# Kernel tuning notes

Measured on AMD Instinct MI355X. Metric: run time of the kernel, lower is better.

Reference implementation:

```python
import jax, jax.numpy as jnp
import numpy as np

NUM_HEADS = 8      # SD1.x UNet cross-attn heads at 64x64 block
NUM_PROMPTS = 4    # batch = 2*NUM_PROMPTS (uncond + cond CFG halves)


def setup_inputs() -> dict:
    key = jax.random.key(0)
    ks = jax.random.split(key, 8)
    B, T, C = 2 * NUM_PROMPTS, 4096, 320   # spatial tokens, inner dim
    S, D = 77, 768                          # CLIP text seq len / width
    return {
        "hidden_states": jax.random.normal(ks[0], (B, T, C), jnp.float32),
        "encoder_hidden_states": jax.random.normal(ks[1], (B, S, D), jnp.float32),
        "mapper": jax.random.uniform(ks[2], (NUM_PROMPTS - 1, S, S), jnp.float32),
        "Wq": jax.random.normal(ks[3], (C, C), jnp.float32) * 0.02,
        "Wk": jax.random.normal(ks[4], (D, C), jnp.float32) * 0.02,
        "Wv": jax.random.normal(ks[5], (D, C), jnp.float32) * 0.02,
        "Wo": jax.random.normal(ks[6], (C, C), jnp.float32) * 0.02,
        "bo": jnp.zeros((C,), jnp.float32),
    }


def reference(hidden_states, encoder_hidden_states, mapper, Wq, Wk, Wv, Wo, bo):
    B, T, C = hidden_states.shape
    S = encoder_hidden_states.shape[1]
    H = NUM_HEADS
    d = C // H
    scale = 1.0 / jnp.sqrt(jnp.asarray(d, hidden_states.dtype))

    # projections + head split (diffusers head_to_batch_dim layout)
    q = (hidden_states @ Wq).reshape(B, T, H, d)
    k = (encoder_hidden_states @ Wk).reshape(B, S, H, d)
    v = (encoder_hidden_states @ Wv).reshape(B, S, H, d)

    # full attention probabilities must be materialized for the P2P swap
    scores = jnp.einsum('bthd,bshd->bhts', q, k) * scale
    probs = jax.nn.softmax(scores, axis=-1)  # [B, H, T, S]

    # conditional (CFG) half: [P, H, T, S]; swap via mapper einsum (cross-attn,
    # cur_step < num_steps_cross branch of swap_attention_probs)
    half = B // 2
    uncond = probs[:half]
    cond = probs[half:]
    attn_base = cond[0]                                   # [H, T, S]
    replaced = jnp.einsum('htm,pme->phte', attn_base, mapper)  # [P-1, H, T, S]
    cond = jnp.concatenate([attn_base[None], replaced], axis=0)
    probs = jnp.concatenate([uncond, cond], axis=0)

    # value matmul + merge heads (batch_to_head_dim) + output projection
    out = jnp.einsum('bhts,bshd->bthd', probs, v).reshape(B, T, C)
    return out @ Wo + bo
```

## Files before the change

kernel.cpp:

```cpp
#include <hip/hip_runtime.h>
#include <hip/hip_bf16.h>

typedef unsigned short ushort;
typedef __attribute__((ext_vector_type(8))) short bf16x8;
typedef __attribute__((ext_vector_type(8))) unsigned short ushort8;
typedef __attribute__((ext_vector_type(4))) float f32x4;
typedef __attribute__((ext_vector_type(4))) float float4v;

__device__ __forceinline__ ushort f2bf(float f) {
    union { float f; unsigned u; } v; v.f = f;
    unsigned r = v.u + 0x7FFFu + ((v.u >> 16) & 1u);
    return (ushort)(r >> 16);
}
__device__ __forceinline__ float bf2f(ushort u) {
    union { unsigned u; float f; } v; v.u = ((unsigned)u) << 16;
    return v.f;
}

#define KF_SZ   (5u * 8 * 5 * 2 * 512)
#define VF_SZ   (5u * 8 * 3 * 3 * 512)
#define VPF_SZ  (3u * 8 * 3 * 3 * 512)
#define WF_SZ   (10u * 2 * 10 * 512)

__global__ __launch_bounds__(256) void prep_k(
    const float* __restrict__ Wq, const float* __restrict__ Wk,
    const float* __restrict__ Wv, const float* __restrict__ Wo,
    ushort* __restrict__ Wq_t, ushort* __restrict__ Wk_t,
    ushort* __restrict__ Wv_t, ushort* __restrict__ Wo_t,
    ushort* __restrict__ Kf, ushort* __restrict__ Vf, ushort* __restrict__ VPf)
{
    int b = blockIdx.x;
    if (b >= 680) {
        const ushort8 z8 = {0,0,0,0,0,0,0,0};
        unsigned i = (b - 680) * 256 + threadIdx.x;
        if (i < KF_SZ / 8) ((ushort8*)Kf)[i] = z8;
        else if (i < (KF_SZ + VF_SZ) / 8) ((ushort8*)Vf)[i - KF_SZ / 8] = z8;
        else if (i < (KF_SZ + VF_SZ + VPF_SZ) / 8) ((ushort8*)VPf)[i - (KF_SZ + VF_SZ) / 8] = z8;
        return;
    }
    __shared__ ushort t[32][33];
    const float* src; ushort* dst; int K; int tb;
    if (b < 100)      { src = Wq; dst = Wq_t; K = 320; tb = b; }
    else if (b < 340) { src = Wk; dst = Wk_t; K = 768; tb = b - 100; }
    else if (b < 580) { src = Wv; dst = Wv_t; K = 768; tb = b - 340; }
    else              { src = Wo; dst = Wo_t; K = 320; tb = b - 580; }
    int tc = tb % 10, tr = tb / 10;
    int tx = threadIdx.x & 31, ty = threadIdx.x >> 5;
    #pragma unroll
    for (int p = 0; p < 4; ++p) {
        int k = tr * 32 + ty + p * 8, n = tc * 32 + tx;
        t[ty + p * 8][tx] = f2bf(src[(size_t)k * 320 + n]);
    }
    __syncthreads();
    #pragma unroll
    for (int p = 0; p < 4; ++p) {
        int n = tc * 32 + ty + p * 8, k = tr * 32 + tx;
        dst[(size_t)n * K + k] = t[tx][ty + p * 8];
    }
}

__global__ __launch_bounds__(256) void gemm_kv(
    const float* __restrict__ E, const ushort* __restrict__ Wk_t,
    const ushort* __restrict__ Wv_t, const ushort* __restrict__ Wq_t,
    const ushort* __restrict__ Wo_t,
    float* __restrict__ part, ushort* __restrict__ Wof, ushort* __restrict__ Wqf)
{
    const int tid = threadIdx.x;
    const int bid = blockIdx.x;
    if (bid >= 160) {
        int i = (bid - 160) * 256 + tid;
        const ushort* src; ushort* dst;
        if (i < 12800) { src = Wo_t; dst = Wof; }
        else           { src = Wq_t; dst = Wqf; i -= 12800; }
        int g = i >> 6, l = i & 63;
        int kk = g / 20, half = (g / 10) & 1, f = g % 10;
        int n = half * 160 + f * 16 + (l & 15);
        int k0 = kk * 32 + (l >> 4) * 8;
        *(ushort8*)(dst + (size_t)g * 512 + l * 8) =
            *(const ushort8*)(src + (size_t)n * 320 + k0);
        return;
    }
    __shared__ ushort A_lds[2][64 * 40];
    __shared__ ushort B_lds[2][320 * 40];
    const int w = tid >> 6, l = tid & 63;
    const int c15 = l & 15, khi = (l >> 4) * 8;
    const int r = tid >> 2, p = (tid & 3) * 8;
    const int rbase = (l >> 4) * 4;
    f32x4 acc[4][5] = {};

    const int mtile = bid % 10, mat = (bid / 10) & 1, ks = bid / 20;
    const int m0 = mtile * 64, kk0 = ks * 96;
    const ushort* Bt = mat ? Wv_t : Wk_t;
    const int m = m0 + r;
    const bool live = (m < 616);
    const float* Abase = E + (size_t)(live ? m : 0) * 768 + p;
    float4v a0 = {0,0,0,0}, a1 = {0,0,0,0};
    ushort8 breg[5];
    if (live) { a0 = *(const float4v*)(Abase + kk0); a1 = *(const float4v*)(Abase + kk0 + 4); }
    #pragma unroll
    for (int i = 0; i < 5; ++i) {
        int idx = tid + i * 256; int n = idx >> 2, q = (idx & 3) * 8;
        breg[i] = *(const ushort8*)(Bt + (size_t)n * 768 + kk0 + q);
    }
    {
        ushort* d = &A_lds[0][r * 40 + p];
        d[0]=f2bf(a0.x); d[1]=f2bf(a0.y); d[2]=f2bf(a0.z); d[3]=f2bf(a0.w);
        d[4]=f2bf(a1.x); d[5]=f2bf(a1.y); d[6]=f2bf(a1.z); d[7]=f2bf(a1.w);
        #pragma unroll
        for (int i = 0; i < 5; ++i) {
            int idx = tid + i * 256; int n = idx >> 2, q = (idx & 3) * 8;
            *(ushort8*)&B_lds[0][n * 40 + q] = breg[i];
        }
    }
    __syncthreads();
    for (int k = 0; k < 3; ++k) {
        const int cur = k & 1;
        if (k < 2) {
            int kk = kk0 + (k + 1) * 32;
            if (live) { a0 = *(const float4v*)(Abase + kk); a1 = *(const float4v*)(Abase + kk + 4); }
            #pragma unroll
            for (int i = 0; i < 5; ++i) {
                int idx = tid + i * 256; int n = idx >> 2, q = (idx & 3) * 8;
                breg[i] = *(const ushort8*)(Bt + (size_t)n * 768 + kk + q);
            }
        }
        bf16x8 a[4];
        #pragma unroll
        for (int mf = 0; mf < 4; ++mf)
            a[mf] = *(const bf16x8*)&A_lds[cur][(mf * 16 + c15) * 40 + khi];
        #pragma unroll
        for (int f = 0; f < 5; ++f) {
            bf16x8 b = *(const bf16x8*)&B_lds[cur][(w * 80 + f * 16 + c15) * 40 + khi];
            #pragma unroll
            for (int mf = 0; mf < 4; ++mf)
                acc[mf][f] = __builtin_amdgcn_mfma_f32_16x16x32_bf16(a[mf], b, acc[mf][f], 0, 0, 0);
        }
        if (k < 2) {
            const int nxt = cur ^ 1;
            ushort* d = &A_lds[nxt][r * 40 + p];
            d[0]=f2bf(a0.x); d[1]=f2bf(a0.y); d[2]=f2bf(a0.z); d[3]=f2bf(a0.w);
            d[4]=f2bf(a1.x); d[5]=f2bf(a1.y); d[6]=f2bf(a1.z); d[7]=f2bf(a1.w);
            #pragma unroll
            for (int i = 0; i < 5; ++i) {
                int idx = tid + i * 256; int n = idx >> 2, q = (idx & 3) * 8;
                *(ushort8*)&B_lds[nxt][n * 40 + q] = breg[i];
            }
            __syncthreads();
        }
    }
    float* dst = part + (size_t)(mat * 8 + ks) * 640 * 320;
    #pragma unroll
    for (int mf = 0; mf < 4; ++mf)
        #pragma unroll
        for (int f = 0; f < 5; ++f) {
            int col = w * 80 + f * 16 + c15;
            #pragma unroll
            for (int rr = 0; rr < 4; ++rr)
                dst[(size_t)(m0 + mf * 16 + rbase + rr) * 320 + col] = acc[mf][f][rr];
        }
}

__global__ __launch_bounds__(256) void kv_reduce(
    const float* __restrict__ part, ushort* __restrict__ Kf,
    ushort* __restrict__ Vf, ushort* __restrict__ VVt)
{
    int idx = blockIdx.x * 256 + threadIdx.x;
    if (idx >= 616 * 320) return;
    int mat = blockIdx.y;
    int row = idx / 320, col = idx - row * 320;
    float s8 = 0.f;
    #pragma unroll
    for (int ks = 0; ks < 8; ++ks)
        s8 += part[((size_t)(mat * 8 + ks) * 640 + row) * 320 + col];
    ushort b = f2bf(s8);
    int bt = row / 77, s = row - bt * 77;
    int h = col / 40, kd = col - h * 40;
    if (mat == 0) {
        if (bt < 5) {
            int kt = kd >> 5, chunk = (kd >> 3) & 3;
            int lane = (s & 15) | (chunk << 4);
            Kf[((size_t)((bt * 8 + h) * 5 + (s >> 4)) * 2 + kt) * 512 + lane * 8 + (kd & 7)] = b;
        }
    } else {
        if (bt < 5) {
            int lane = (kd & 15) | (((s >> 3) & 3) << 4);
            Vf[(((size_t)(bt * 8 + h) * 3 + (kd >> 4)) * 3 + (s >> 5)) * 512 + lane * 8 + (s & 7)] = b;
        } else {
            VVt[((size_t)bt * 320 + col) * 80 + s] = b;
        }
    }
}

__global__ void vprime_k(const float* __restrict__ mapper, const ushort* __restrict__ VVt,
                         ushort* __restrict__ VPf)
{
    int pm = blockIdx.x;
    int p = pm / 77, m = pm - p * 77;
    __shared__ float mp[77];
    int tid = threadIdx.x;
    if (tid < 77) mp[tid] = mapper[(size_t)pm * 77 + tid];
    __syncthreads();
    const ushort* vrow = VVt + ((size_t)(5 + p) * 320 + tid) * 80;
    float acc = 0.f;
    for (int e = 0; e < 77; ++e) acc += mp[e] * bf2f(vrow[e]);
    int h = tid / 40, dc = tid - h * 40;
    int lane = (dc & 15) | (((m >> 3) & 3) << 4);
    VPf[(((size_t)(p * 8 + h) * 3 + (dc >> 4)) * 3 + (m >> 5)) * 512 + lane * 8 + (m & 7)] = f2bf(acc);
}

#define ATT_SCALE 0.15811388300841897f
__global__ __launch_bounds__(512, 4) void attn_out_k(
    const float* __restrict__ hs, const ushort* __restrict__ Wqf,
    const ushort* __restrict__ Kf, const ushort* __restrict__ Vf,
    const ushort* __restrict__ VPf, const ushort* __restrict__ Wof,
    const float* __restrict__ bias, float* __restrict__ out)
{
    __shared__ __align__(16) ushort AO_lds[64 * 328];
    __shared__ __align__(16) ushort P_lds[8 * 16 * 104];
    ushort* W_lds = P_lds;

    const int tid = threadIdx.x;
    const int ww = tid >> 6, l = tid & 63;
    const int c15 = l & 15, hi4 = l >> 4;
    const int khi = hi4 * 8, rbase = hi4 * 4;
    const int bt = blockIdx.y, t0 = blockIdx.x * 64;
    const int qb = (bt < 5) ? bt : 4;
    const ushort* Vfb = (bt < 5) ? (Vf + (size_t)bt * (8 * 3 * 3 * 512))
                                 : (VPf + (size_t)(bt - 5) * (8 * 3 * 3 * 512));
    const ushort8 z8 = {0,0,0,0,0,0,0,0};
    ushort* Pw = P_lds + ww * (16 * 104);
    const int rg = ww & 3, half = ww >> 2;
    const int cb = half * 160;

    for (int i = tid; i < 2560; i += 512) {
        int r = i / 40, cc = i - (i / 40) * 40;
        const float4v* s = (const float4v*)(hs + (size_t)(qb * 4096 + t0 + r) * 320 + cc * 8);
        float4v x0 = s[0], x1 = s[1];
        ushort* d = &AO_lds[r * 328 + cc * 8];
        d[0]=f2bf(x0.x); d[1]=f2bf(x0.y); d[2]=f2bf(x0.z); d[3]=f2bf(x0.w);
        d[4]=f2bf(x1.x); d[5]=f2bf(x1.y); d[6]=f2bf(x1.z); d[7]=f2bf(x1.w);
    }
    __syncthreads();

    {
        f32x4 qacc[10] = {};
        for (int kk = 0; kk < 10; ++kk) {
            const ushort* wsrc = Wqf + (size_t)kk * 10240;
            int c0 = tid, c1 = tid + 512, c2 = tid + 1024;
            *(ushort8*)&W_lds[c0 * 8] = *(const ushort8*)(wsrc + c0 * 8);
            *(ushort8*)&W_lds[c1 * 8] = *(const ushort8*)(wsrc + c1 * 8);
            if (c2 < 1280) *(ushort8*)&W_lds[c2 * 8] = *(const ushort8*)(wsrc + c2 * 8);
            __syncthreads();
            bf16x8 a = *(const bf16x8*)&AO_lds[(rg * 16 + c15) * 328 + kk * 32 + khi];
            #pragma unroll
            for (int f = 0; f < 10; ++f) {
                bf16x8 b = *(const bf16x8*)&W_lds[(half * 10 + f) * 512 + l * 8];
                qacc[f] = __builtin_amdgcn_mfma_f32_16x16x32_bf16(a, b, qacc[f], 0, 0, 0);
            }
            __syncthreads();
        }
        #pragma unroll
        for (int f = 0; f < 10; ++f) {
            int col = cb + f * 16 + c15;
            #pragma unroll
            for (int rr = 0; rr < 4; ++rr)
                AO_lds[(rg * 16 + rbase + rr) * 328 + col] = f2bf(qacc[f][rr]);
        }
    }
    __syncthreads();

    const int h = ww;
    if (l < 48) {
        int r = l / 3, c = l - 3 * (l / 3);
        *(ushort8*)&Pw[r * 104 + 80 + c * 8] = z8;
    }
    bf16x8 kreg[5][2];
    #pragma unroll
    for (int f = 0; f < 5; ++f) {
        const ushort* kfb = Kf + ((size_t)((qb * 8 + h) * 5 + f) * 2) * 512 + l * 8;
        kreg[f][0] = *(const bf16x8*)(kfb);
        kreg[f][1] = *(const bf16x8*)(kfb + 512);
    }

    for (int rg4 = 0; rg4 < 4; ++rg4) {
        bf16x8 qa0 = *(const bf16x8*)&AO_lds[(rg4 * 16 + c15) * 328 + h * 40 + khi];
        bf16x8 qa1 = {0,0,0,0,0,0,0,0};
        if (hi4 == 0) qa1 = *(const bf16x8*)&AO_lds[(rg4 * 16 + c15) * 328 + h * 40 + 32];

        f32x4 sacc[5] = {};
        #pragma unroll
        for (int f = 0; f < 5; ++f) {
            sacc[f] = __builtin_amdgcn_mfma_f32_16x16x32_bf16(qa0, kreg[f][0], sacc[f], 0, 0, 0);
            sacc[f] = __builtin_amdgcn_mfma_f32_16x16x32_bf16(qa1, kreg[f][1], sacc[f], 0, 0, 0);
        }

        float pv[5][4];
        #pragma unroll
        for (int r = 0; r < 4; ++r) {
            float sum = 0.f;
            #pragma unroll
            for (int f = 0; f < 5; ++f) {
                bool valid = (f < 4) || (c15 < 13);
                float e = valid ? __expf(sacc[f][r] * ATT_SCALE) : 0.f;
                pv[f][r] = e; sum += e;
            }
            #pragma unroll
            for (int d = 1; d < 16; d <<= 1) sum += __shfl_xor(sum, d);
            float inv = 1.f / sum;
            #pragma unroll
            for (int f = 0; f < 5; ++f) pv[f][r] *= inv;
        }

        #pragma unroll
        for (int r = 0; r < 4; ++r)
            #pragma unroll
            for (int f = 0; f < 5; ++f)
                Pw[(rbase + r) * 104 + f * 16 + c15] = f2bf(pv[f][r]);

        bf16x8 pa[3];
        #pragma unroll
        for (int kt = 0; kt < 3; ++kt)
            pa[kt] = *(const bf16x8*)&Pw[c15 * 104 + kt * 32 + khi];
        f32x4 oacc[3];
        #pragma unroll
        for (int f = 0; f < 3; ++f) {
            bf16x8 v0 = *(const bf16x8*)(Vfb + (((size_t)(h * 3 + f) * 3 + 0)) * 512 + l * 8);
            bf16x8 v1 = *(const bf16x8*)(Vfb + (((size_t)(h * 3 + f) * 3 + 1)) * 512 + l * 8);
            bf16x8 v2 = *(const bf16x8*)(Vfb + (((size_t)(h * 3 + f) * 3 + 2)) * 512 + l * 8);
            f32x4 o = {};
            o = __builtin_amdgcn_mfma_f32_16x16x32_bf16(pa[0], v0, o, 0, 0, 0);
            o = __builtin_amdgcn_mfma_f32_16x16x32_bf16(pa[1], v1, o, 0, 0, 0);
            o = __builtin_amdgcn_mfma_f32_16x16x32_bf16(pa[2], v2, o, 0, 0, 0);
            oacc[f] = o;
        }

        #pragma unroll
        for (int f = 0; f < 3; ++f) {
            int col = f * 16 + c15;
            if (col < 40) {
                #pragma unroll
                for (int r = 0; r < 4; ++r)
                    AO_lds[(rg4 * 16 + rbase + r) * 328 + h * 40 + col] = f2bf(oacc[f][r]);
            }
        }
    }
    __syncthreads();

    f32x4 acc[10] = {};
    for (int kk = 0; kk < 10; ++kk) {
        const ushort* wsrc = Wof + (size_t)kk * 10240;
        {
            int c0 = tid, c1 = tid + 512, c2 = tid + 1024;
            *(ushort8*)&W_lds[c0 * 8] = *(const ushort8*)(wsrc + c0 * 8);
            *(ushort8*)&W_lds[c1 * 8] = *(const ushort8*)(wsrc + c1 * 8);
            if (c2 < 1280) *(ushort8*)&W_lds[c2 * 8] = *(const ushort8*)(wsrc + c2 * 8);
        }
        __syncthreads();
        bf16x8 a = *(const bf16x8*)&AO_lds[(rg * 16 + c15) * 328 + kk * 32 + khi];
        #pragma unroll
        for (int f = 0; f < 10; ++f) {
            bf16x8 b = *(const bf16x8*)&W_lds[(half * 10 + f) * 512 + l * 8];
            acc[f] = __builtin_amdgcn_mfma_f32_16x16x32_bf16(a, b, acc[f], 0, 0, 0);
        }
        if (kk < 9) __syncthreads();
    }

    #pragma unroll
    for (int f = 0; f < 10; ++f) {
        int col = cb + f * 16 + c15;
        #pragma unroll
        for (int rr = 0; rr < 4; ++rr)
            out[(size_t)(bt * 4096 + t0 + rg * 16 + rbase + rr) * 320 + col]
                = acc[f][rr] + bias[col];
    }
}

extern "C" void kernel_launch(void* const* d_in, const int* in_sizes, int n_in,
                              void* d_out, int out_size, void* d_ws, size_t ws_size,
                              hipStream_t stream) {
    (void)in_sizes; (void)n_in; (void)out_size; (void)ws_size;
    const float* hs     = (const float*)d_in[0];
    const float* ehs    = (const float*)d_in[1];
    const float* mapper = (const float*)d_in[2];
    const float* Wq     = (const float*)d_in[3];
    const float* Wk     = (const float*)d_in[4];
    const float* Wv     = (const float*)d_in[5];
    const float* Wo     = (const float*)d_in[6];
    const float* bo     = (const float*)d_in[7];
    float* out = (float*)d_out;

    ushort* ws   = (ushort*)d_ws;
    ushort* Wq_t = ws;
    ushort* Wk_t = Wq_t + 320 * 320;
    ushort* Wv_t = Wk_t + 320 * 768;
    ushort* Wo_t = Wv_t + 320 * 768;
    ushort* Wof  = Wo_t + 320 * 320;
    ushort* Wqf  = Wof + WF_SZ;
    ushort* Kfb  = Wqf + WF_SZ;
    ushort* Vfb  = Kfb + KF_SZ;
    ushort* VPfb = Vfb + VF_SZ;
    ushort* VVt  = VPfb + VPF_SZ;
    float*  part = (float*)(VVt + 8 * 320 * 80);

    prep_k<<<1069, 256, 0, stream>>>(Wq, Wk, Wv, Wo, Wq_t, Wk_t, Wv_t, Wo_t,
                                     Kfb, Vfb, VPfb);
    gemm_kv<<<260, 256, 0, stream>>>(ehs, Wk_t, Wv_t, Wq_t, Wo_t, part, Wof, Wqf);
    kv_reduce<<<dim3(770, 2), 256, 0, stream>>>(part, Kfb, Vfb, VVt);
    vprime_k<<<231, 320, 0, stream>>>(mapper, VVt, VPfb);
    attn_out_k<<<dim3(64, 8), 512, 0, stream>>>(hs, Wqf, Kfb, Vfb, VPfb, Wof, bo, out);
}
```

Measured before the change: 65.65 us.

## Load Q/O projection weights directly from global into registers, retile warps 2x4

The Q and output projection GEMMs no longer stage weight tiles through LDS with per-k barriers. Each warp now covers 32 rows by 80 columns, reading B fragments straight from global memory in a re-laid-out weight format and reusing each fragment across two row fragments. This removes 20 block-wide barriers and LDS traffic per projection. The cost is that weight reads now depend on L2/global latency with no LDS sharing across warps. The P padding zeroing is moved earlier because LDS is no longer reused for weights.

```diff
diff --git a/kernel.cpp b/kernel.cpp
--- a/kernel.cpp
+++ b/kernel.cpp
@@ -20,7 +20,7 @@
 #define KF_SZ   (5u * 8 * 5 * 2 * 512)
 #define VF_SZ   (5u * 8 * 3 * 3 * 512)
 #define VPF_SZ  (3u * 8 * 3 * 3 * 512)
-#define WF_SZ   (10u * 2 * 10 * 512)
+#define WF_SZ   (10u * 4 * 5 * 512)
 
 __global__ __launch_bounds__(256) void prep_k(
     const float* __restrict__ Wq, const float* __restrict__ Wk,
@@ -73,8 +73,8 @@
         if (i < 12800) { src = Wo_t; dst = Wof; }
         else           { src = Wq_t; dst = Wqf; i -= 12800; }
         int g = i >> 6, l = i & 63;
-        int kk = g / 20, half = (g / 10) & 1, f = g % 10;
-        int n = half * 160 + f * 16 + (l & 15);
+        int kk = g / 20, cg = (g / 5) & 3, f = g % 5;
+        int n = cg * 80 + f * 16 + (l & 15);
         int k0 = kk * 32 + (l >> 4) * 8;
         *(ushort8*)(dst + (size_t)g * 512 + l * 8) =
             *(const ushort8*)(src + (size_t)n * 320 + k0);
@@ -217,7 +217,6 @@
 {
     __shared__ __align__(16) ushort AO_lds[64 * 328];
     __shared__ __align__(16) ushort P_lds[8 * 16 * 104];
-    ushort* W_lds = P_lds;
 
     const int tid = threadIdx.x;
     const int ww = tid >> 6, l = tid & 63;
@@ -229,8 +228,12 @@
                                  : (VPf + (size_t)(bt - 5) * (8 * 3 * 3 * 512));
     const ushort8 z8 = {0,0,0,0,0,0,0,0};
     ushort* Pw = P_lds + ww * (16 * 104);
-    const int rg = ww & 3, half = ww >> 2;
-    const int cb = half * 160;
+    const int rp = ww & 1, cg = ww >> 1;
+
+    if (l < 48) {
+        int r = l / 3, c = l - 3 * (l / 3);
+        *(ushort8*)&Pw[r * 104 + 80 + c * 8] = z8;
+    }
 
     for (int i = tid; i < 2560; i += 512) {
         int r = i / 40, cc = i - (i / 40) * 40;
@@ -243,37 +246,32 @@
     __syncthreads();
 
     {
-        f32x4 qacc[10] = {};
+        f32x4 qacc[2][5] = {};
         for (int kk = 0; kk < 10; ++kk) {
-            const ushort* wsrc = Wqf + (size_t)kk * 10240;
-            int c0 = tid, c1 = tid + 512, c2 = tid + 1024;
-            *(ushort8*)&W_lds[c0 * 8] = *(const ushort8*)(wsrc + c0 * 8);
-            *(ushort8*)&W_lds[c1 * 8] = *(const ushort8*)(wsrc + c1 * 8);
-            if (c2 < 1280) *(ushort8*)&W_lds[c2 * 8] = *(const ushort8*)(wsrc + c2 * 8);
-            __syncthreads();
-            bf16x8 a = *(const bf16x8*)&AO_lds[(rg * 16 + c15) * 328 + kk * 32 + khi];
-            #pragma unroll
-            for (int f = 0; f < 10; ++f) {
-                bf16x8 b = *(const bf16x8*)&W_lds[(half * 10 + f) * 512 + l * 8];
-                qacc[f] = __builtin_amdgcn_mfma_f32_16x16x32_bf16(a, b, qacc[f], 0, 0, 0);
-            }
-            __syncthreads();
-        }
-        #pragma unroll
-        for (int f = 0; f < 10; ++f) {
-            int col = cb + f * 16 + c15;
-            #pragma unroll
-            for (int rr = 0; rr < 4; ++rr)
-                AO_lds[(rg * 16 + rbase + rr) * 328 + col] = f2bf(qacc[f][rr]);
-        }
+            bf16x8 a0 = *(const bf16x8*)&AO_lds[(rp * 32 + c15) * 328 + kk * 32 + khi];
+            bf16x8 a1 = *(const bf16x8*)&AO_lds[(rp * 32 + 16 + c15) * 328 + kk * 32 + khi];
+            const ushort* wb = Wqf + (size_t)((kk * 4 + cg) * 5) * 512 + l * 8;
+            #pragma unroll
+            for (int f = 0; f < 5; ++f) {
+                bf16x8 b = *(const bf16x8*)(wb + (size_t)f * 512);
+                qacc[0][f] = __builtin_amdgcn_mfma_f32_16x16x32_bf16(a0, b, qacc[0][f], 0, 0, 0);
+                qacc[1][f] = __builtin_amdgcn_mfma_f32_16x16x32_bf16(a1, b, qacc[1][f], 0, 0, 0);
+            }
+        }
+        __syncthreads();
+        #pragma unroll
+        for (int mf = 0; mf < 2; ++mf)
+            #pragma unroll
+            for (int f = 0; f < 5; ++f) {
+                int col = cg * 80 + f * 16 + c15;
+                #pragma unroll
+                for (int rr = 0; rr < 4; ++rr)
+                    AO_lds[(rp * 32 + mf * 16 + rbase + rr) * 328 + col] = f2bf(qacc[mf][f][rr]);
+            }
     }
     __syncthreads();
 
     const int h = ww;
-    if (l < 48) {
-        int r = l / 3, c = l - 3 * (l / 3);
-        *(ushort8*)&Pw[r * 104 + 80 + c * 8] = z8;
-    }
     bf16x8 kreg[5][2];
     #pragma unroll
     for (int f = 0; f < 5; ++f) {
@@ -346,33 +344,29 @@
     }
     __syncthreads();
 
-    f32x4 acc[10] = {};
+    f32x4 acc[2][5] = {};
     for (int kk = 0; kk < 10; ++kk) {
-        const ushort* wsrc = Wof + (size_t)kk * 10240;
-        {
-            int c0 = tid, c1 = tid + 512, c2 = tid + 1024;
-            *(ushort8*)&W_lds[c0 * 8] = *(const ushort8*)(wsrc + c0 * 8);
-            *(ushort8*)&W_lds[c1 * 8] = *(const ushort8*)(wsrc + c1 * 8);
-            if (c2 < 1280) *(ushort8*)&W_lds[c2 * 8] = *(const ushort8*)(wsrc + c2 * 8);
-        }
-        __syncthreads();
-        bf16x8 a = *(const bf16x8*)&AO_lds[(rg * 16 + c15) * 328 + kk * 32 + khi];
-        #pragma unroll
-        for (int f = 0; f < 10; ++f) {
-            bf16x8 b = *(const bf16x8*)&W_lds[(half * 10 + f) * 512 + l * 8];
-            acc[f] = __builtin_amdgcn_mfma_f32_16x16x32_bf16(a, b, acc[f], 0, 0, 0);
-        }
-        if (kk < 9) __syncthreads();
-    }
-
-    #pragma unroll
-    for (int f = 0; f < 10; ++f) {
-        int col = cb + f * 16 + c15;
-        #pragma unroll
-        for (int rr = 0; rr < 4; ++rr)
-            out[(size_t)(bt * 4096 + t0 + rg * 16 + rbase + rr) * 320 + col]
-                = acc[f][rr] + bias[col];
-    }
+        bf16x8 a0 = *(const bf16x8*)&AO_lds[(rp * 32 + c15) * 328 + kk * 32 + khi];
+        bf16x8 a1 = *(const bf16x8*)&AO_lds[(rp * 32 + 16 + c15) * 328 + kk * 32 + khi];
+        const ushort* wb = Wof + (size_t)((kk * 4 + cg) * 5) * 512 + l * 8;
+        #pragma unroll
+        for (int f = 0; f < 5; ++f) {
+            bf16x8 b = *(const bf16x8*)(wb + (size_t)f * 512);
+            acc[0][f] = __builtin_amdgcn_mfma_f32_16x16x32_bf16(a0, b, acc[0][f], 0, 0, 0);
+            acc[1][f] = __builtin_amdgcn_mfma_f32_16x16x32_bf16(a1, b, acc[1][f], 0, 0, 0);
+        }
+    }
+
+    #pragma unroll
+    for (int mf = 0; mf < 2; ++mf)
+        #pragma unroll
+        for (int f = 0; f < 5; ++f) {
+            int col = cg * 80 + f * 16 + c15;
+            #pragma unroll
+            for (int rr = 0; rr < 4; ++rr)
+                out[(size_t)(bt * 4096 + t0 + rp * 32 + mf * 16 + rbase + rr) * 320 + col]
+                    = acc[mf][f][rr] + bias[col];
+        }
 }
 
 extern "C" void kernel_launch(void* const* d_in, const int* in_sizes, int n_in,
```

Result: slower. 71.06 us (+8.2%).
